# Optimization experiments

Hardware: AMD Instinct MI355X
Metric: run time of the kernel (lower is better)

The kernel has to match this reference:

```python
import jax, jax.numpy as jnp
import numpy as np

DIM = 384
HEADS = 12
AGENT = 49
POOL = 7  # int(sqrt(AGENT))


def setup_inputs() -> dict:
    key = jax.random.key(0)
    ks = jax.random.split(key, 9)
    b, c, h, w = 32, DIM, 56, 56
    x = jax.random.normal(ks[0], (b, c, h, w), dtype=jnp.float32)
    qkv_w = jax.random.normal(ks[1], (c, 3 * c), dtype=jnp.float32) * 0.02
    qkv_b = jnp.zeros((3 * c,), dtype=jnp.float32)
    proj_w = jax.random.normal(ks[2], (c, c), dtype=jnp.float32) * 0.02
    proj_b = jnp.zeros((c,), dtype=jnp.float32)
    an_bias = jax.random.normal(ks[3], (HEADS, AGENT, 7, 7), dtype=jnp.float32) * 0.02
    na_bias = jax.random.normal(ks[4], (HEADS, AGENT, 7, 7), dtype=jnp.float32) * 0.02
    dwc_w = jax.random.normal(ks[5], (c, 1, 3, 3), dtype=jnp.float32) * 0.1
    dwc_b = jnp.zeros((c,), dtype=jnp.float32)
    return {"x": x, "qkv_w": qkv_w, "qkv_b": qkv_b, "proj_w": proj_w,
            "proj_b": proj_b, "an_bias": an_bias, "na_bias": na_bias,
            "dwc_w": dwc_w, "dwc_b": dwc_b}


def agent_attention(x, qkv_w, qkv_b, proj_w, proj_b, an_bias, na_bias, dwc_w, dwc_b):
    b, c, h, w = x.shape
    n = h * w
    H = HEADS
    hd = c // H
    scale = hd ** -0.5

    shortcut = x
    xf = x.reshape(b, c, n).transpose(0, 2, 1)            # [b, n, c]
    qkv = xf @ qkv_w + qkv_b                              # [b, n, 3c]
    q, k, v = jnp.split(qkv, 3, axis=-1)                  # each [b, n, c]

    # agent tokens: adaptive avg pool of q over uniform (h//POOL, w//POOL) windows
    q_img = q.reshape(b, h, w, c)
    agent = q_img.reshape(b, POOL, h // POOL, POOL, w // POOL, c).mean(axis=(2, 4))
    agent = agent.reshape(b, AGENT, c)

    # split heads -> [b, H, n, hd] / [b, H, AGENT, hd]
    qh = q.reshape(b, n, H, hd).transpose(0, 2, 1, 3)
    kh = k.reshape(b, n, H, hd).transpose(0, 2, 1, 3)
    vh = v.reshape(b, n, H, hd).transpose(0, 2, 1, 3)
    ah = agent.reshape(b, AGENT, H, hd).transpose(0, 2, 1, 3)

    # stage 1: agent tokens attend to keys (pos bias bilinearly upsampled 7x7 -> h x w)
    pb1 = jax.image.resize(an_bias, (H, AGENT, h, w), method='bilinear')
    pb1 = pb1.reshape(1, H, AGENT, n)
    agent_attn = jax.nn.softmax(
        jnp.einsum('bhad,bhnd->bhan', ah * scale, kh) + pb1, axis=-1)
    agent_v = jnp.einsum('bhan,bhnd->bhad', agent_attn, vh)  # [b, H, AGENT, hd]

    # stage 2: queries attend to agent tokens
    ab1 = jax.image.resize(na_bias, (H, AGENT, h, w), method='bilinear')
    ab1 = ab1.reshape(1, H, AGENT, n).transpose(0, 1, 3, 2)  # [1, H, n, AGENT]
    q_attn = jax.nn.softmax(
        jnp.einsum('bhnd,bhad->bhna', qh * scale, ah) + ab1, axis=-1)
    o = jnp.einsum('bhna,bhad->bhnd', q_attn, agent_v)       # [b, H, n, hd]
    o = o.transpose(0, 2, 1, 3).reshape(b, n, c)

    # depthwise 3x3 conv on v (NCHW), residual add
    v_img = v.reshape(b, h, w, c).transpose(0, 3, 1, 2)      # [b, c, h, w]
    dw = jax.lax.conv_general_dilated(
        v_img, dwc_w, window_strides=(1, 1), padding='SAME',
        feature_group_count=c, dimension_numbers=('NCHW', 'OIHW', 'NCHW'))
    dw = dw + dwc_b[None, :, None, None]
    o = o + dw.transpose(0, 2, 3, 1).reshape(b, n, c)

    o = o @ proj_w + proj_b                                  # [b, n, c]
    o = o.reshape(b, h, w, c).transpose(0, 3, 1, 2)          # [b, c, h, w]
    return shortcut * jax.nn.sigmoid(o)


def reference(x, qkv_w, qkv_b, proj_w, proj_b, an_bias, na_bias, dwc_w, dwc_b):
    return agent_attention(x, qkv_w, qkv_b, proj_w, proj_b,
                           an_bias, na_bias, dwc_w, dwc_b)
```

## Files before the change

kernel.cpp:

```cpp
#include <hip/hip_runtime.h>

#define DIM    384
#define HEADS  12
#define NPIX   3136
#define BATCH  32
#define AGENTS 49
#define HD     32

typedef unsigned short u16;
typedef unsigned int   u32;
typedef __attribute__((ext_vector_type(8))) short short8;
typedef __attribute__((ext_vector_type(4))) float f32x4;

__device__ __forceinline__ float bf2f(u16 u) { return __uint_as_float(((u32)u) << 16); }
__device__ __forceinline__ u16 f2bf(float f) {
    u32 i = __float_as_uint(f);
    u32 r = i + 0x7fffu + ((i >> 16) & 1u);
    return (u16)(r >> 16);
}

__device__ __forceinline__ void unpack_row32(const u16* p, float* f) {
    const uint4* q = (const uint4*)p;
#pragma unroll
    for (int i = 0; i < 4; i++) {
        uint4 u = q[i];
        u32 w0 = u.x, w1 = u.y, w2 = u.z, w3 = u.w;
        f[i*8+0] = __uint_as_float(w0 << 16); f[i*8+1] = __uint_as_float(w0 & 0xffff0000u);
        f[i*8+2] = __uint_as_float(w1 << 16); f[i*8+3] = __uint_as_float(w1 & 0xffff0000u);
        f[i*8+4] = __uint_as_float(w2 << 16); f[i*8+5] = __uint_as_float(w2 & 0xffff0000u);
        f[i*8+6] = __uint_as_float(w3 << 16); f[i*8+7] = __uint_as_float(w3 & 0xffff0000u);
    }
}

__global__ __launch_bounds__(256) void transpose_mat(const float* __restrict__ src, u16* __restrict__ dst,
                                                     int R, int C) {
    __shared__ u16 tile[64][65];
    int c0 = blockIdx.x * 64, r0 = blockIdx.y * 64;
    int t0 = threadIdx.x & 63, t1 = threadIdx.x >> 6;
#pragma unroll
    for (int i = 0; i < 16; i++) {
        int r = t1 + i*4;
        tile[t0][r] = f2bf(src[(size_t)(r0 + r)*C + c0 + t0]);
    }
    __syncthreads();
#pragma unroll
    for (int i = 0; i < 16; i++) {
        int c = t1 + i*4;
        dst[(size_t)(c0 + c)*R + r0 + t0] = tile[c][t0];
    }
}

__global__ __launch_bounds__(256) void convert_x(const float* __restrict__ x, u16* __restrict__ xT) {
    __shared__ float tile[64][65];
    const int p0 = blockIdx.x * 64;
    const int c0 = blockIdx.y * 64;
    const int b  = blockIdx.z;
    const int t0 = threadIdx.x & 63, t1 = threadIdx.x >> 6;
#pragma unroll
    for (int i = 0; i < 16; i++) {
        int ch = t1 + i*4;
        tile[t0][ch] = x[((size_t)b*DIM + c0 + ch)*NPIX + p0 + t0];
    }
    __syncthreads();
    const int cb = threadIdx.x & 7, r = threadIdx.x >> 3;
#pragma unroll
    for (int half = 0; half < 2; half++) {
        int rr = r + half*32;
        const float* tp = &tile[rr][cb*8];
        u32 w0 = f2bf(tp[0]) | ((u32)f2bf(tp[1]) << 16);
        u32 w1 = f2bf(tp[2]) | ((u32)f2bf(tp[3]) << 16);
        u32 w2 = f2bf(tp[4]) | ((u32)f2bf(tp[5]) << 16);
        u32 w3 = f2bf(tp[6]) | ((u32)f2bf(tp[7]) << 16);
        *(uint4*)&xT[((size_t)b*NPIX + p0 + rr)*DIM + c0 + cb*8] = make_uint4(w0, w1, w2, w3);
    }
}

__global__ __launch_bounds__(256) void upsample_bias(const float* __restrict__ src, float* __restrict__ dst) {
    int idx = blockIdx.x * 256 + threadIdx.x;
    int xo = idx % 56; int t = idx / 56;
    int yo = t % 56;   int ha = t / 56;
    float fy = yo * 0.125f - 0.4375f;
    float fx = xo * 0.125f - 0.4375f;
    float y0f = floorf(fy), x0f = floorf(fx);
    float wy = fy - y0f, wx = fx - x0f;
    int y0 = (int)y0f, x0 = (int)x0f;
    int y0c = max(y0, 0), y1c = min(y0 + 1, 6);
    int x0c = max(x0, 0), x1c = min(x0 + 1, 6);
    const float* sp = src + (size_t)ha * 49;
    float v00 = sp[y0c*7 + x0c], v01 = sp[y0c*7 + x1c];
    float v10 = sp[y1c*7 + x0c], v11 = sp[y1c*7 + x1c];
    dst[idx] = (1.f-wy)*((1.f-wx)*v00 + wx*v01) + wy*((1.f-wx)*v10 + wx*v11);
}

__global__ __launch_bounds__(256) void zero_init(float* __restrict__ p, int n) {
    int i = blockIdx.x * 256 + threadIdx.x;
    if (i < n) p[i] = 0.f;
}

__device__ __forceinline__ void mfma_tile(const short* As, const short* Bs, f32x4 acc[4][4],
                                          int wm, int wn, int quad, int lr) {
#pragma unroll
    for (int ks = 0; ks < 2; ks++) {
        int g = ks*4 + quad;
        short8 af[4], bg[4];
#pragma unroll
        for (int im = 0; im < 4; im++) {
            int r = wm*64 + im*16 + lr;
            af[im] = *(const short8*)&As[r*64 + ((g ^ (r & 7)) << 3)];
        }
#pragma unroll
        for (int in_ = 0; in_ < 4; in_++) {
            int r = wn*64 + in_*16 + lr;
            bg[in_] = *(const short8*)&Bs[r*64 + ((g ^ (r & 7)) << 3)];
        }
#pragma unroll
        for (int im = 0; im < 4; im++)
#pragma unroll
            for (int in_ = 0; in_ < 4; in_++)
                acc[im][in_] = __builtin_amdgcn_mfma_f32_16x16x32_bf16(af[im], bg[in_], acc[im][in_], 0, 0, 0);
    }
}

__global__ __launch_bounds__(256) void gemm_qkv(const u16* __restrict__ xT, const u16* __restrict__ Bw,
                                                const float* __restrict__ bias,
                                                u16* __restrict__ qb, u16* __restrict__ kb, u16* __restrict__ vb) {
    __shared__ __align__(16) short As[128*64];
    __shared__ __align__(16) short Bs[128*64];
    f32x4 acc[4][4] = {};
    const int l  = blockIdx.x + 9*(blockIdx.y + 25*blockIdx.z);
    const int k8 = l & 7, j = l >> 3;
    const int c  = (j/9)*8 + k8;
    const int i9 = j - (j/9)*9;
    const int n0 = i9 * 128;
    const int p0 = (c % 25) * 128;
    const int bb = c / 25;
    const int tid  = threadIdx.x;
    const int lane = tid & 63, wave = tid >> 6;
    const int wm = wave >> 1, wn = wave & 1;
    const int quad = lane >> 4, lr = lane & 15;

    for (int kt = 0; kt < DIM; kt += 64) {
        __syncthreads();
#pragma unroll
        for (int c2 = 0; c2 < 4; c2++) {
            int idx = c2*256 + tid;
            int r = idx >> 3, g = idx & 7;
            int so = r*64 + ((g ^ (r & 7)) << 3);
            *(uint4*)&As[so] = *(const uint4*)&xT[((size_t)bb*NPIX + p0 + r)*DIM + kt + g*8];
            *(uint4*)&Bs[so] = *(const uint4*)&Bw[(size_t)(n0 + r)*DIM + kt + g*8];
        }
        __syncthreads();
        mfma_tile(As, Bs, acc, wm, wn, quad, lr);
    }
#pragma unroll
    for (int in_ = 0; in_ < 4; in_++) {
        int col = n0 + wn*64 + in_*16 + lr;
        int which = col / 384;
        int ch = col - which*384;
        int head = ch >> 5, d = ch & 31;
        float bcol = bias[col];
        u16* dstp = (which == 0) ? qb : ((which == 1) ? kb : vb);
#pragma unroll
        for (int im = 0; im < 4; im++) {
            int prow = p0 + wm*64 + im*16 + quad*4;
#pragma unroll
            for (int r = 0; r < 4; r++) {
                int pix = prow + r;
                if (pix < NPIX) {
                    float v = acc[im][in_][r] + bcol;
                    dstp[((size_t)(bb*HEADS + head)*NPIX + pix)*HD + d] = f2bf(v);
                }
            }
        }
    }
}

__global__ __launch_bounds__(256) void gemm_proj(const u16* __restrict__ A, const u16* __restrict__ Bw,
                                                 const float* __restrict__ bias, const float* __restrict__ xin,
                                                 float* __restrict__ outp) {
    __shared__ __align__(16) short As[128*64];
    __shared__ __align__(16) short Bs[128*64];
    f32x4 acc[4][4] = {};
    const int l  = blockIdx.x + 3*blockIdx.y;
    const int k8 = l & 7, j = l >> 3;
    const int c  = (j/3)*8 + k8;
    const int i3 = j - (j/3)*3;
    const int n0 = i3*128, m0 = c*128;
    const int tid  = threadIdx.x;
    const int lane = tid & 63, wave = tid >> 6;
    const int wm = wave >> 1, wn = wave & 1;
    const int quad = lane >> 4, lr = lane & 15;
    for (int kt = 0; kt < DIM; kt += 64) {
        __syncthreads();
#pragma unroll
        for (int c2 = 0; c2 < 4; c2++) {
            int idx = c2*256 + tid;
            int r = idx >> 3, g = idx & 7;
            int so = r*64 + ((g ^ (r & 7)) << 3);
            *(uint4*)&As[so] = *(const uint4*)&A[(size_t)(m0 + r)*DIM + kt + g*8];
            *(uint4*)&Bs[so] = *(const uint4*)&Bw[(size_t)(n0 + r)*DIM + kt + g*8];
        }
        __syncthreads();
        mfma_tile(As, Bs, acc, wm, wn, quad, lr);
    }
#pragma unroll
    for (int in_ = 0; in_ < 4; in_++) {
        int col = n0 + wn*64 + in_*16 + lr;
        float bcol = bias[col];
#pragma unroll
        for (int im = 0; im < 4; im++) {
            int rowb = m0 + wm*64 + im*16 + quad*4;
#pragma unroll
            for (int r = 0; r < 4; r++) {
                int grow = rowb + r;
                int bb = grow / NPIX;
                int pix = grow - bb*NPIX;
                float o = acc[im][in_][r] + bcol;
                float sg = 1.f / (1.f + __expf(-o));
                size_t xi = ((size_t)bb*DIM + col)*NPIX + pix;
                outp[xi] = xin[xi] * sg;
            }
        }
    }
}

__global__ __launch_bounds__(256) void pool_q(const u16* __restrict__ qb, float* __restrict__ agent) {
    int gt = blockIdx.x * 256 + threadIdx.x;
    int d = gt & 31;
    int t2 = gt >> 5;
    int a = t2 % 49;
    int bh = t2 / 49;
    int ay = a / 7, ax = a % 7;
    const u16* qp = qb + (size_t)bh*NPIX*HD + d;
    float s = 0.f;
#pragma unroll
    for (int dy = 0; dy < 8; dy++)
#pragma unroll
        for (int dx = 0; dx < 8; dx++)
            s += bf2f(qp[(size_t)((ay*8 + dy)*56 + ax*8 + dx)*HD]);
    agent[gt] = s * (1.f/64.f);
}

#define S1_CHUNK  224
#define S1_NCHUNK 14
#define S1_PSTR   228

__global__ __launch_bounds__(256) void stage1_part(const u16* __restrict__ kb, const u16* __restrict__ vb,
                                                   const float* __restrict__ agent, const float* __restrict__ pb1,
                                                   float* __restrict__ accv, float* __restrict__ accl) {
    __shared__ __align__(16) float ah_s[AGENTS*HD];
    __shared__ __align__(16) float P_s[AGENTS*S1_PSTR];
    const int chunk = blockIdx.x;
    const int bh    = blockIdx.y;
    const int hh    = bh % HEADS;
    const int tid   = threadIdx.x;
    const int pix0  = chunk * S1_CHUNK;
    const float scale = 0.1767766952966369f;

    for (int i = tid; i < AGENTS*HD; i += 256)
        ah_s[i] = agent[(size_t)bh*AGENTS*HD + i];
    __syncthreads();

    if (tid < S1_CHUNK) {
        float kf[32];
        unpack_row32(kb + ((size_t)bh*NPIX + pix0 + tid)*HD, kf);
        const float* pbp = pb1 + (size_t)hh*AGENTS*NPIX + pix0 + tid;
        for (int a = 0; a < AGENTS; a++) {
            const float* ap = &ah_s[a*HD];
            float s0 = 0.f, s1 = 0.f, s2 = 0.f, s3 = 0.f;
#pragma unroll
            for (int d = 0; d < 32; d += 4) {
                s0 = fmaf(ap[d+0], kf[d+0], s0);
                s1 = fmaf(ap[d+1], kf[d+1], s1);
                s2 = fmaf(ap[d+2], kf[d+2], s2);
                s3 = fmaf(ap[d+3], kf[d+3], s3);
            }
            float s = ((s0+s1)+(s2+s3))*scale + pbp[(size_t)a*NPIX];
            P_s[a*S1_PSTR + tid] = __expf(s);
        }
    }
    __syncthreads();

    if (tid < 196) {
        int a = tid >> 2, sub = tid & 3;
        const float* pp = &P_s[a*S1_PSTR + sub*56];
        float ls = 0.f;
        for (int k = 0; k < 56; k++) ls += pp[k];
        ls += __shfl_xor(ls, 1, 64);
        ls += __shfl_xor(ls, 2, 64);
        if (sub == 0) atomicAdd(&accl[(size_t)bh*AGENTS + a], ls);
    }

    const int d = tid & 31, g = tid >> 5;
    float acc[AGENTS];
#pragma unroll
    for (int a = 0; a < AGENTS; a++) acc[a] = 0.f;
    const u16* vp = vb + ((size_t)bh*NPIX + pix0)*HD + d;
    for (int p8 = 0; p8 < 7; p8++) {
        int pixl = p8*32 + g*4;
        float v0 = bf2f(vp[(size_t)(pixl+0)*HD]);
        float v1 = bf2f(vp[(size_t)(pixl+1)*HD]);
        float v2 = bf2f(vp[(size_t)(pixl+2)*HD]);
        float v3 = bf2f(vp[(size_t)(pixl+3)*HD]);
#pragma unroll
        for (int a = 0; a < AGENTS; a++) {
            f32x4 pq = *(const f32x4*)&P_s[a*S1_PSTR + pixl];
            acc[a] = fmaf(pq[0], v0, fmaf(pq[1], v1, fmaf(pq[2], v2, fmaf(pq[3], v3, acc[a]))));
        }
    }
    __syncthreads();

#pragma unroll
    for (int a = 0; a < AGENTS; a++) acc[a] += __shfl_xor(acc[a], 32, 64);
    float* red = (float*)P_s;
    const int w = tid >> 6;
    if ((tid & 63) < 32) {
#pragma unroll
        for (int a = 0; a < AGENTS; a++) red[(w*AGENTS + a)*HD + d] = acc[a];
    }
    __syncthreads();
    for (int i = tid; i < AGENTS*HD; i += 256) {
        float s = red[i] + red[AGENTS*HD + i] + red[2*AGENTS*HD + i] + red[3*AGENTS*HD + i];
        atomicAdd(&accv[(size_t)bh*AGENTS*HD + i], s);
    }
}

__global__ __launch_bounds__(256) void stage1_final(const float* __restrict__ accv, const float* __restrict__ accl,
                                                    float* __restrict__ agentv) {
    int i = blockIdx.x * 256 + threadIdx.x;
    agentv[i] = accv[i] / accl[i >> 5];
}

__global__ __launch_bounds__(256) void stage2(const u16* __restrict__ qb, const float* __restrict__ agent,
                                              const float* __restrict__ agentv, const float* __restrict__ ab1,
                                              u16* __restrict__ obuf) {
    __shared__ float ah_s[AGENTS*32];
    __shared__ float av_s[AGENTS*32];
    const int b = blockIdx.z, hh = blockIdx.y, chunk = blockIdx.x;
    const int bh = b*HEADS + hh;
    for (int i = threadIdx.x; i < AGENTS*32; i += 256) {
        ah_s[i] = agent[(size_t)bh*AGENTS*HD + i];
        av_s[i] = agentv[(size_t)bh*AGENTS*HD + i];
    }
    __syncthreads();
    int pix = chunk*256 + threadIdx.x;
    if (pix >= NPIX) return;
    const float scale = 0.1767766952966369f;
    float qf[32];
    unpack_row32(qb + ((size_t)bh*NPIX + pix)*HD, qf);
    float oacc[32];
#pragma unroll
    for (int d = 0; d < 32; d++) oacc[d] = 0.f;
    float l = 0.f;
    const float* abp = ab1 + (size_t)hh*AGENTS*NPIX + pix;
    for (int a = 0; a < AGENTS; a++) {
        float s = 0.f;
#pragma unroll
        for (int d = 0; d < 32; d++) s = fmaf(qf[d], ah_s[a*32 + d], s);
        s = s * scale + abp[(size_t)a*NPIX];
        float p = __expf(s);
        l += p;
#pragma unroll
        for (int d = 0; d < 32; d++) oacc[d] = fmaf(p, av_s[a*32 + d], oacc[d]);
    }
    float inv = 1.f / l;
    u16* op = obuf + ((size_t)b*NPIX + pix)*DIM + hh*HD;
#pragma unroll
    for (int d2 = 0; d2 < 16; d2++) {
        u32 lo = f2bf(oacc[2*d2] * inv);
        u32 hi = f2bf(oacc[2*d2 + 1] * inv);
        ((u32*)op)[d2] = lo | (hi << 16);
    }
}

__global__ __launch_bounds__(256) void dwconv_add(const u16* __restrict__ vb, const float* __restrict__ dwcw,
                                                  const float* __restrict__ dwcb, u16* __restrict__ obuf) {
    const int chunk = blockIdx.x;
    const int hh = blockIdx.y, b = blockIdx.z;
    const int dd = threadIdx.x & 31, pg = threadIdx.x >> 5;
    const int ch = hh*HD + dd;
    float wgt[9];
#pragma unroll
    for (int i = 0; i < 9; i++) wgt[i] = dwcw[ch*9 + i];
    float bbias = dwcb[ch];
    const u16* vp = vb + (size_t)(b*HEADS + hh)*NPIX*HD + dd;
#pragma unroll
    for (int i = 0; i < 4; i++) {
        int pix = chunk*32 + i*8 + pg;
        int y = pix / 56, x0 = pix - y*56;
        float s = bbias;
#pragma unroll
        for (int dy = 0; dy < 3; dy++) {
            int yy = y + dy - 1;
            if (yy < 0 || yy > 55) continue;
#pragma unroll
            for (int dx = 0; dx < 3; dx++) {
                int xx = x0 + dx - 1;
                if (xx < 0 || xx > 55) continue;
                s = fmaf(wgt[dy*3 + dx], bf2f(vp[(size_t)(yy*56 + xx)*HD]), s);
            }
        }
        size_t oi = ((size_t)b*NPIX + pix)*DIM + ch;
        obuf[oi] = f2bf(bf2f(obuf[oi]) + s);
    }
}

extern "C" void kernel_launch(void* const* d_in, const int* in_sizes, int n_in,
                              void* d_out, int out_size, void* d_ws, size_t ws_size,
                              hipStream_t stream) {
    const float* x     = (const float*)d_in[0];
    const float* qkvw  = (const float*)d_in[1];
    const float* qkvb  = (const float*)d_in[2];
    const float* projw = (const float*)d_in[3];
    const float* projb = (const float*)d_in[4];
    const float* anb   = (const float*)d_in[5];
    const float* nab   = (const float*)d_in[6];
    const float* dwcw  = (const float*)d_in[7];
    const float* dwcb  = (const float*)d_in[8];
    float* out = (float*)d_out;

    char* w = (char*)d_ws;
    const size_t SZ_BNC = (size_t)BATCH*NPIX*DIM*2;
    u16* qb     = (u16*)w;  w += SZ_BNC;
    u16* kb     = (u16*)w;  w += SZ_BNC;
    u16* vb     = (u16*)w;  w += SZ_BNC;
    u16* qkvwT  = (u16*)w;  w += (size_t)1152*384*2;
    u16* projwT = (u16*)w;  w += (size_t)384*384*2;
    u16* obuf   = kb;

    char* o = (char*)d_out;
    float* pb1    = (float*)o; o += (size_t)HEADS*AGENTS*NPIX*4;
    float* ab1    = (float*)o; o += (size_t)HEADS*AGENTS*NPIX*4;
    float* agent  = (float*)o; o += (size_t)BATCH*HEADS*AGENTS*HD*4;
    float* agentv = (float*)o; o += (size_t)BATCH*HEADS*AGENTS*HD*4;
    float* accv   = (float*)o; o += (size_t)BATCH*HEADS*AGENTS*HD*4;
    float* accl   = (float*)o; o += (size_t)BATCH*HEADS*AGENTS*4;
    u16*   xT     = (u16*)o;   o += SZ_BNC;

    const int nacc = BATCH*HEADS*AGENTS*(HD + 1);

    convert_x    <<<dim3(49, 6, 32), 256, 0, stream>>>(x, xT);
    transpose_mat<<<dim3(18, 6),     256, 0, stream>>>(qkvw, qkvwT, 384, 1152);
    transpose_mat<<<dim3(6, 6),      256, 0, stream>>>(projw, projwT, 384, 384);
    upsample_bias<<<dim3(7203),      256, 0, stream>>>(anb, pb1);
    upsample_bias<<<dim3(7203),      256, 0, stream>>>(nab, ab1);
    zero_init    <<<dim3((nacc + 255)/256), 256, 0, stream>>>(accv, nacc);
    gemm_qkv     <<<dim3(9, 25, 32), 256, 0, stream>>>(xT, qkvwT, qkvb, qb, kb, vb);
    pool_q       <<<dim3(2352),      256, 0, stream>>>(qb, agent);
    stage1_part  <<<dim3(S1_NCHUNK, BATCH*HEADS), 256, 0, stream>>>(kb, vb, agent, pb1, accv, accl);
    stage1_final <<<dim3(2352),      256, 0, stream>>>(accv, accl, agentv);
    stage2       <<<dim3(13, 12, 32),256, 0, stream>>>(qb, agent, agentv, ab1, obuf);
    dwconv_add   <<<dim3(98, 12, 32),256, 0, stream>>>(vb, dwcw, dwcb, obuf);
    gemm_proj    <<<dim3(3, 784),    256, 0, stream>>>(obuf, projwT, projb, x, out);
}
```

Baseline: 1.360 ms.

## Double-buffer QKV and projection GEMM tiles with direct global-to-LDS loads

Both bf16 GEMM kernels now stage tiles with global_load_lds, which writes global data straight into LDS and skips the register round trip. The LDS buffers are doubled so the next K-tile is prefetched while MFMAs run on the current one, leaving one barrier per iteration. The XOR swizzle moves from the LDS destination to the global source column so the existing swizzled read pattern still holds. This doubles LDS use per block (64KB), which may cut occupancy, and the prefetch relies on a single barrier to guard buffer reuse.

New measurement: 1.348 ms. About the same (-0.9%).

```diff
diff --git a/kernel.cpp b/kernel.cpp
--- a/kernel.cpp
+++ b/kernel.cpp
@@ -17,6 +17,11 @@
     u32 i = __float_as_uint(f);
     u32 r = i + 0x7fffu + ((i >> 16) & 1u);
     return (u16)(r >> 16);
+}
+
+__device__ __forceinline__ void glds16(const void* g, void* l) {
+    __builtin_amdgcn_global_load_lds((const __attribute__((address_space(1))) void*)g,
+                                     (__attribute__((address_space(3))) void*)l, 16, 0, 0);
 }
 
 __device__ __forceinline__ void unpack_row32(const u16* p, float* f) {
@@ -124,8 +129,8 @@
 __global__ __launch_bounds__(256) void gemm_qkv(const u16* __restrict__ xT, const u16* __restrict__ Bw,
                                                 const float* __restrict__ bias,
                                                 u16* __restrict__ qb, u16* __restrict__ kb, u16* __restrict__ vb) {
-    __shared__ __align__(16) short As[128*64];
-    __shared__ __align__(16) short Bs[128*64];
+    __shared__ __align__(16) short As[2][128*64];
+    __shared__ __align__(16) short Bs[2][128*64];
     f32x4 acc[4][4] = {};
     const int l  = blockIdx.x + 9*(blockIdx.y + 25*blockIdx.z);
     const int k8 = l & 7, j = l >> 3;
@@ -138,20 +143,33 @@
     const int lane = tid & 63, wave = tid >> 6;
     const int wm = wave >> 1, wn = wave & 1;
     const int quad = lane >> 4, lr = lane & 15;
-
-    for (int kt = 0; kt < DIM; kt += 64) {
+    const int rsub = lane >> 3;
+    const int gsrc = (lane & 7) ^ rsub;
+
+    const u16* arow = xT + ((size_t)bb*NPIX + p0 + rsub)*DIM + gsrc*8;
+    const u16* brow = Bw + ((size_t)(n0 + rsub))*DIM + gsrc*8;
+
+#define QKV_STAGE(b2, kt)                                                       \
+    {                                                                           \
+        _Pragma("unroll")                                                       \
+        for (int cc = 0; cc < 4; cc++) {                                        \
+            int rowb = cc*32 + wave*8;                                          \
+            glds16(arow + (size_t)rowb*DIM + (kt), &As[b2][rowb*64]);           \
+            glds16(brow + (size_t)rowb*DIM + (kt), &Bs[b2][rowb*64]);           \
+        }                                                                       \
+    }
+
+    QKV_STAGE(0, 0);
+    __syncthreads();
+    int buf = 0;
+    for (int t = 0; t < 6; t++) {
+        if (t < 5) QKV_STAGE(buf ^ 1, (t + 1)*64);
+        mfma_tile(As[buf], Bs[buf], acc, wm, wn, quad, lr);
         __syncthreads();
-#pragma unroll
-        for (int c2 = 0; c2 < 4; c2++) {
-            int idx = c2*256 + tid;
-            int r = idx >> 3, g = idx & 7;
-            int so = r*64 + ((g ^ (r & 7)) << 3);
-            *(uint4*)&As[so] = *(const uint4*)&xT[((size_t)bb*NPIX + p0 + r)*DIM + kt + g*8];
-            *(uint4*)&Bs[so] = *(const uint4*)&Bw[(size_t)(n0 + r)*DIM + kt + g*8];
-        }
-        __syncthreads();
-        mfma_tile(As, Bs, acc, wm, wn, quad, lr);
-    }
+        buf ^= 1;
+    }
+#undef QKV_STAGE
+
 #pragma unroll
     for (int in_ = 0; in_ < 4; in_++) {
         int col = n0 + wn*64 + in_*16 + lr;
@@ -178,8 +196,8 @@
 __global__ __launch_bounds__(256) void gemm_proj(const u16* __restrict__ A, const u16* __restrict__ Bw,
                                                  const float* __restrict__ bias, const float* __restrict__ xin,
                                                  float* __restrict__ outp) {
-    __shared__ __align__(16) short As[128*64];
-    __shared__ __align__(16) short Bs[128*64];
+    __shared__ __align__(16) short As[2][128*64];
+    __shared__ __align__(16) short Bs[2][128*64];
     f32x4 acc[4][4] = {};
     const int l  = blockIdx.x + 3*blockIdx.y;
     const int k8 = l & 7, j = l >> 3;
@@ -190,19 +208,33 @@
     const int lane = tid & 63, wave = tid >> 6;
     const int wm = wave >> 1, wn = wave & 1;
     const int quad = lane >> 4, lr = lane & 15;
-    for (int kt = 0; kt < DIM; kt += 64) {
+    const int rsub = lane >> 3;
+    const int gsrc = (lane & 7) ^ rsub;
+
+    const u16* arow = A  + ((size_t)(m0 + rsub))*DIM + gsrc*8;
+    const u16* brow = Bw + ((size_t)(n0 + rsub))*DIM + gsrc*8;
+
+#define PROJ_STAGE(b2, kt)                                                      \
+    {                                                                           \
+        _Pragma("unroll")                                                       \
+        for (int cc = 0; cc < 4; cc++) {                                        \
+            int rowb = cc*32 + wave*8;                                          \
+            glds16(arow + (size_t)rowb*DIM + (kt), &As[b2][rowb*64]);           \
+            glds16(brow + (size_t)rowb*DIM + (kt), &Bs[b2][rowb*64]);           \
+        }                                                                       \
+    }
+
+    PROJ_STAGE(0, 0);
+    __syncthreads();
+    int buf = 0;
+    for (int t = 0; t < 6; t++) {
+        if (t < 5) PROJ_STAGE(buf ^ 1, (t + 1)*64);
+        mfma_tile(As[buf], Bs[buf], acc, wm, wn, quad, lr);
         __syncthreads();
-#pragma unroll
-        for (int c2 = 0; c2 < 4; c2++) {
-            int idx = c2*256 + tid;
-            int r = idx >> 3, g = idx & 7;
-            int so = r*64 + ((g ^ (r & 7)) << 3);
-            *(uint4*)&As[so] = *(const uint4*)&A[(size_t)(m0 + r)*DIM + kt + g*8];
-            *(uint4*)&Bs[so] = *(const uint4*)&Bw[(size_t)(n0 + r)*DIM + kt + g*8];
-        }
-        __syncthreads();
-        mfma_tile(As, Bs, acc, wm, wn, quad, lr);
-    }
+        buf ^= 1;
+    }
+#undef PROJ_STAGE
+
 #pragma unroll
     for (int in_ = 0; in_ < 4; in_++) {
         int col = n0 + wn*64 + in_*16 + lr;
```
